# Performance work log

Measured on AMD Instinct MI355X. Metric: run time of the kernel, lower is better.

The kernel has to match this reference:

```python
import jax, jax.numpy as jnp
import numpy as np

RES = 1024
FEAT = 12
CB = 32
H_IMG, W_IMG = 1080, 1920


def cube_sample(cubemap, d):
    """Cube-map bilinear texture sample (nvdiffrast-style face selection,
    clamped bilinear within the selected face).
    cubemap: [6, R, R, C], d: [N, 3] unit directions -> [N, C]."""
    R = cubemap.shape[1]
    x, y, z = d[:, 0], d[:, 1], d[:, 2]
    ax, ay, az = jnp.abs(x), jnp.abs(y), jnp.abs(z)
    is_x = (ax >= ay) & (ax >= az)
    is_y = (~is_x) & (ay >= az)
    face = jnp.where(is_x, jnp.where(x >= 0, 0, 1),
           jnp.where(is_y, jnp.where(y >= 0, 2, 3),
                     jnp.where(z >= 0, 4, 5)))
    ma = jnp.where(is_x, ax, jnp.where(is_y, ay, az))
    u = jnp.where(is_x, jnp.where(x >= 0, -z, z),
        jnp.where(is_y, x, jnp.where(z >= 0, x, -x)))
    v = jnp.where(is_x, -y, jnp.where(is_y, jnp.where(y >= 0, z, -z), -y))
    eps = 1e-9
    s = (u / (ma + eps) + 1.0) * 0.5 * R - 0.5  # texel-space column
    t = (v / (ma + eps) + 1.0) * 0.5 * R - 0.5  # texel-space row
    x0 = jnp.floor(s); y0 = jnp.floor(t)
    fx = (s - x0)[:, None]; fy = (t - y0)[:, None]
    x0i = jnp.clip(x0.astype(jnp.int32), 0, R - 1)
    x1i = jnp.clip(x0i + 1, 0, R - 1)
    y0i = jnp.clip(y0.astype(jnp.int32), 0, R - 1)
    y1i = jnp.clip(y0i + 1, 0, R - 1)
    c00 = cubemap[face, y0i, x0i]
    c01 = cubemap[face, y0i, x1i]
    c10 = cubemap[face, y1i, x0i]
    c11 = cubemap[face, y1i, x1i]
    return (c00 * (1 - fx) + c01 * fx) * (1 - fy) + (c10 * (1 - fx) + c11 * fx) * fy


def setup_inputs() -> dict:
    key = jax.random.key(0)
    ks = jax.random.split(key, 9)
    rays_d = jax.random.normal(ks[0], (H_IMG, W_IMG, 3), jnp.float32)
    rays_d = rays_d / jnp.linalg.norm(rays_d, axis=-1, keepdims=True)
    mask = jax.random.randint(ks[1], (H_IMG, W_IMG), 0, 2) > 0  # sky mask
    sky_cube_map = jax.random.normal(ks[2], (6, RES, RES, FEAT), jnp.float32) * 0.1
    sky_codebook = jax.random.normal(ks[3], (CB, FEAT), jnp.float32) * 0.1
    W1 = jax.random.normal(ks[4], (FEAT + 3, 32), jnp.float32) * 0.25
    b1 = jnp.zeros((32,), jnp.float32)
    W2 = jax.random.normal(ks[5], (32, 32), jnp.float32) * 0.18
    b2 = jnp.zeros((32,), jnp.float32)
    W3 = jax.random.normal(ks[6], (32, 3), jnp.float32) * 0.18
    b3 = jnp.zeros((3,), jnp.float32)
    return {"rays_d": rays_d, "mask": mask, "sky_cube_map": sky_cube_map,
            "sky_codebook": sky_codebook, "W1": W1, "b1": b1,
            "W2": W2, "b2": b2, "W3": W3, "b3": b3}


def reference(rays_d, mask, sky_cube_map, sky_codebook, W1, b1, W2, b2, W3, b3):
    H, W = mask.shape
    d = rays_d.reshape(-1, 3)                       # [N, 3]
    feat_enc = cube_sample(sky_cube_map, d)         # [N, 12]
    # vq_st with detached codebook: nearest-codeword quantize, straight-through.
    cb = jax.lax.stop_gradient(sky_codebook)
    d2 = (jnp.sum(feat_enc * feat_enc, -1, keepdims=True)
          - 2.0 * (feat_enc @ cb.T)
          + jnp.sum(cb * cb, -1))                   # [N, 32]
    idx = jnp.argmin(d2, axis=-1)                   # [N]
    q = feat_enc + jax.lax.stop_gradient(cb[idx] - feat_enc)
    h = jnp.concatenate([q, d], axis=-1)            # [N, 15]
    h = jax.nn.relu(h @ W1 + b1)
    h = jax.nn.relu(h @ W2 + b2)
    rgb = jax.nn.sigmoid(h @ W3 + b3)               # [N, 3]
    # scatter shaded sky color into the (black-background) buffer via the mask
    img = jnp.where(mask.reshape(-1)[:, None], rgb, 0.0)
    return jnp.clip(img.reshape(H, W, 3).transpose(2, 0, 1), 0.0, 1.0)
```

## Files before the change

kernel.cpp:

```cpp
#include <hip/hip_runtime.h>
#include <math.h>

#define RES   1024
#define FEATC 12
#define CBN   32
#define H_IMG 1080
#define W_IMG 1920
#define NPIX  (H_IMG * W_IMG)

__global__ __launch_bounds__(256) void sky_kernel(
    const float* __restrict__ rays_d,
    const int*   __restrict__ mask,
    const float* __restrict__ cube,
    const float* __restrict__ cb,
    const float* __restrict__ W1,
    const float* __restrict__ b1,
    const float* __restrict__ W2,
    const float* __restrict__ b2,
    const float* __restrict__ W3,
    const float* __restrict__ b3,
    float*       __restrict__ out)
{
    __shared__ float sW1[15 * 32];
    __shared__ float sb1[32];
    __shared__ float sW2[32 * 32];
    __shared__ float sb2[32];
    __shared__ float sW3[32 * 3];
    __shared__ float sb3[3];
    __shared__ float sCB[CBN * FEATC];

    for (int t = threadIdx.x; t < 15 * 32; t += blockDim.x) sW1[t] = W1[t];
    for (int t = threadIdx.x; t < 32;      t += blockDim.x) sb1[t] = b1[t];
    for (int t = threadIdx.x; t < 32 * 32; t += blockDim.x) sW2[t] = W2[t];
    for (int t = threadIdx.x; t < 32;      t += blockDim.x) sb2[t] = b2[t];
    for (int t = threadIdx.x; t < 32 * 3;  t += blockDim.x) sW3[t] = W3[t];
    for (int t = threadIdx.x; t < 3;       t += blockDim.x) sb3[t] = b3[t];
    for (int t = threadIdx.x; t < CBN * FEATC; t += blockDim.x) sCB[t] = cb[t];
    __syncthreads();

    const int i = blockIdx.x * blockDim.x + threadIdx.x;
    if (i >= NPIX) return;

    if (mask[i] == 0) {
        out[0 * NPIX + i] = 0.0f;
        out[1 * NPIX + i] = 0.0f;
        out[2 * NPIX + i] = 0.0f;
        return;
    }

    const float x = rays_d[3 * i + 0];
    const float y = rays_d[3 * i + 1];
    const float z = rays_d[3 * i + 2];

    const float ax = fabsf(x), ay = fabsf(y), az = fabsf(z);
    const bool is_x = (ax >= ay) && (ax >= az);
    const bool is_y = (!is_x) && (ay >= az);

    int face; float ma, u, v;
    if (is_x) {
        face = (x >= 0.0f) ? 0 : 1;
        ma = ax;
        u = (x >= 0.0f) ? -z : z;
        v = -y;
    } else if (is_y) {
        face = (y >= 0.0f) ? 2 : 3;
        ma = ay;
        u = x;
        v = (y >= 0.0f) ? z : -z;
    } else {
        face = (z >= 0.0f) ? 4 : 5;
        ma = az;
        u = (z >= 0.0f) ? x : -x;
        v = -y;
    }

    const float denom = __fadd_rn(ma, 1e-9f);
    const float s = __fsub_rn(__fmul_rn(__fmul_rn(__fadd_rn(__fdiv_rn(u, denom), 1.0f), 0.5f), (float)RES), 0.5f);
    const float t = __fsub_rn(__fmul_rn(__fmul_rn(__fadd_rn(__fdiv_rn(v, denom), 1.0f), 0.5f), (float)RES), 0.5f);

    const float x0f = floorf(s);
    const float y0f = floorf(t);
    const float fx = __fsub_rn(s, x0f);
    const float fy = __fsub_rn(t, y0f);

    int x0i = (int)x0f; x0i = min(max(x0i, 0), RES - 1);
    int x1i = min(x0i + 1, RES - 1);
    int y0i = (int)y0f; y0i = min(max(y0i, 0), RES - 1);
    int y1i = min(y0i + 1, RES - 1);

    const size_t fbase = (size_t)face * RES * RES;
    const size_t off00 = (fbase + (size_t)y0i * RES + x0i) * FEATC;
    const size_t off01 = (fbase + (size_t)y0i * RES + x1i) * FEATC;
    const size_t off10 = (fbase + (size_t)y1i * RES + x0i) * FEATC;
    const size_t off11 = (fbase + (size_t)y1i * RES + x1i) * FEATC;

    const float4* p00 = (const float4*)(cube + off00);
    const float4* p01 = (const float4*)(cube + off01);
    const float4* p10 = (const float4*)(cube + off10);
    const float4* p11 = (const float4*)(cube + off11);

    float c00[FEATC], c01[FEATC], c10[FEATC], c11[FEATC];
    #pragma unroll
    for (int q4 = 0; q4 < 3; ++q4) {
        float4 a = p00[q4]; c00[4*q4+0]=a.x; c00[4*q4+1]=a.y; c00[4*q4+2]=a.z; c00[4*q4+3]=a.w;
        float4 b = p01[q4]; c01[4*q4+0]=b.x; c01[4*q4+1]=b.y; c01[4*q4+2]=b.z; c01[4*q4+3]=b.w;
        float4 c = p10[q4]; c10[4*q4+0]=c.x; c10[4*q4+1]=c.y; c10[4*q4+2]=c.z; c10[4*q4+3]=c.w;
        float4 dd= p11[q4]; c11[4*q4+0]=dd.x;c11[4*q4+1]=dd.y;c11[4*q4+2]=dd.z;c11[4*q4+3]=dd.w;
    }

    const float omfx = __fsub_rn(1.0f, fx);
    const float omfy = __fsub_rn(1.0f, fy);
    float feat[FEATC];
    #pragma unroll
    for (int k = 0; k < FEATC; ++k) {
        const float top = __fadd_rn(__fmul_rn(c00[k], omfx), __fmul_rn(c01[k], fx));
        const float bot = __fadd_rn(__fmul_rn(c10[k], omfx), __fmul_rn(c11[k], fx));
        feat[k] = __fadd_rn(__fmul_rn(top, omfy), __fmul_rn(bot, fy));
    }

    int best = 0;
    double bestd = 1e300;
    for (int j = 0; j < CBN; ++j) {
        double d2 = 0.0;
        #pragma unroll
        for (int k = 0; k < FEATC; ++k) {
            const double diff = (double)feat[k] - (double)sCB[j * FEATC + k];
            d2 += diff * diff;
        }
        if (d2 < bestd) { bestd = d2; best = j; }
    }

    float hin[15];
    #pragma unroll
    for (int k = 0; k < FEATC; ++k)
        hin[k] = __fadd_rn(feat[k], __fsub_rn(sCB[best * FEATC + k], feat[k]));
    hin[12] = x; hin[13] = y; hin[14] = z;

    float h1[32];
    #pragma unroll
    for (int k = 0; k < 32; ++k) {
        float a = sb1[k];
        #pragma unroll
        for (int j = 0; j < 15; ++j) a += hin[j] * sW1[j * 32 + k];
        h1[k] = fmaxf(a, 0.0f);
    }

    float h2[32];
    #pragma unroll
    for (int k = 0; k < 32; ++k) {
        float a = sb2[k];
        #pragma unroll
        for (int j = 0; j < 32; ++j) a += h1[j] * sW2[j * 32 + k];
        h2[k] = fmaxf(a, 0.0f);
    }

    #pragma unroll
    for (int c = 0; c < 3; ++c) {
        float a = sb3[c];
        #pragma unroll
        for (int j = 0; j < 32; ++j) a += h2[j] * sW3[j * 3 + c];
        float r = 1.0f / (1.0f + expf(-a));
        r = fminf(fmaxf(r, 0.0f), 1.0f);
        out[(size_t)c * NPIX + i] = r;
    }
}

extern "C" void kernel_launch(void* const* d_in, const int* in_sizes, int n_in,
                              void* d_out, int out_size, void* d_ws, size_t ws_size,
                              hipStream_t stream) {
    const float* rays_d = (const float*)d_in[0];
    const int*   mask   = (const int*)d_in[1];
    const float* cube   = (const float*)d_in[2];
    const float* cb     = (const float*)d_in[3];
    const float* W1     = (const float*)d_in[4];
    const float* b1     = (const float*)d_in[5];
    const float* W2     = (const float*)d_in[6];
    const float* b2     = (const float*)d_in[7];
    const float* W3     = (const float*)d_in[8];
    const float* b3     = (const float*)d_in[9];
    float* out = (float*)d_out;

    const int block = 256;
    const int grid = (NPIX + block - 1) / block;
    sky_kernel<<<grid, block, 0, stream>>>(rays_d, mask, cube, cb,
                                           W1, b1, W2, b2, W3, b3, out);
}
```

Before: 618.2 us.

## Compact masked pixels into an active list before shading to remove divergence

Adds a prep pass that zeroes background pixels and appends active pixel indices to a workspace list using a global atomic counter. A persistent grid-stride kernel then shades only the listed pixels, so wavefronts no longer idle on half-masked lanes. The codebook search is also changed to a dot-product form with precomputed squared norms in double, and the MLP loops are reordered to an outer-product style. The costs are two extra launches, heavy contention on a single atomic, loss of memory coalescing because list order is scrambled, and a possible change in argmin tie behaviour.

```diff
diff --git a/kernel.cpp b/kernel.cpp
--- a/kernel.cpp
+++ b/kernel.cpp
@@ -8,26 +8,180 @@
 #define W_IMG 1920
 #define NPIX  (H_IMG * W_IMG)
 
-__global__ __launch_bounds__(256) void sky_kernel(
+
+__device__ __forceinline__ void face_uv(float x, float y, float z,
+                                        int& face, float& ma, float& u, float& v)
+{
+    const float ax = fabsf(x), ay = fabsf(y), az = fabsf(z);
+    const bool is_x = (ax >= ay) && (ax >= az);
+    const bool is_y = (!is_x) && (ay >= az);
+    if (is_x) {
+        face = (x >= 0.0f) ? 0 : 1;
+        ma = ax; u = (x >= 0.0f) ? -z : z; v = -y;
+    } else if (is_y) {
+        face = (y >= 0.0f) ? 2 : 3;
+        ma = ay; u = x; v = (y >= 0.0f) ? z : -z;
+    } else {
+        face = (z >= 0.0f) ? 4 : 5;
+        ma = az; u = (z >= 0.0f) ? x : -x; v = -y;
+    }
+}
+
+__device__ __forceinline__ void shade_pixel(
+    int i,
     const float* __restrict__ rays_d,
-    const int*   __restrict__ mask,
+    const float* __restrict__ cube,
+    const float* sW1, const float* sb1,
+    const float* sW2, const float* sb2,
+    const float* sW3, const float* sb3,
+    const float* sCB, const double* sCN,
+    float* __restrict__ out)
+{
+    const float x = rays_d[3 * i + 0];
+    const float y = rays_d[3 * i + 1];
+    const float z = rays_d[3 * i + 2];
+
+    int face; float ma, u, v;
+    face_uv(x, y, z, face, ma, u, v);
+
+    const float denom = __fadd_rn(ma, 1e-9f);
+    const float s = __fsub_rn(__fmul_rn(__fmul_rn(__fadd_rn(__fdiv_rn(u, denom), 1.0f), 0.5f), (float)RES), 0.5f);
+    const float t = __fsub_rn(__fmul_rn(__fmul_rn(__fadd_rn(__fdiv_rn(v, denom), 1.0f), 0.5f), (float)RES), 0.5f);
+
+    const float x0f = floorf(s);
+    const float y0f = floorf(t);
+    const float fx = __fsub_rn(s, x0f);
+    const float fy = __fsub_rn(t, y0f);
+
+    int x0i = (int)x0f; x0i = min(max(x0i, 0), RES - 1);
+    int x1i = min(x0i + 1, RES - 1);
+    int y0i = (int)y0f; y0i = min(max(y0i, 0), RES - 1);
+    int y1i = min(y0i + 1, RES - 1);
+
+    const size_t fbase = (size_t)face * RES * RES;
+    const float4* p00 = (const float4*)(cube + (fbase + (size_t)y0i * RES + x0i) * FEATC);
+    const float4* p01 = (const float4*)(cube + (fbase + (size_t)y0i * RES + x1i) * FEATC);
+    const float4* p10 = (const float4*)(cube + (fbase + (size_t)y1i * RES + x0i) * FEATC);
+    const float4* p11 = (const float4*)(cube + (fbase + (size_t)y1i * RES + x1i) * FEATC);
+
+    float c00[FEATC], c01[FEATC], c10[FEATC], c11[FEATC];
+    #pragma unroll
+    for (int q4 = 0; q4 < 3; ++q4) {
+        float4 a = p00[q4]; c00[4*q4+0]=a.x; c00[4*q4+1]=a.y; c00[4*q4+2]=a.z; c00[4*q4+3]=a.w;
+        float4 b = p01[q4]; c01[4*q4+0]=b.x; c01[4*q4+1]=b.y; c01[4*q4+2]=b.z; c01[4*q4+3]=b.w;
+        float4 c = p10[q4]; c10[4*q4+0]=c.x; c10[4*q4+1]=c.y; c10[4*q4+2]=c.z; c10[4*q4+3]=c.w;
+        float4 dd= p11[q4]; c11[4*q4+0]=dd.x;c11[4*q4+1]=dd.y;c11[4*q4+2]=dd.z;c11[4*q4+3]=dd.w;
+    }
+
+    const float omfx = __fsub_rn(1.0f, fx);
+    const float omfy = __fsub_rn(1.0f, fy);
+    float feat[FEATC];
+    double featd[FEATC];
+    #pragma unroll
+    for (int k = 0; k < FEATC; ++k) {
+        const float top = __fadd_rn(__fmul_rn(c00[k], omfx), __fmul_rn(c01[k], fx));
+        const float bot = __fadd_rn(__fmul_rn(c10[k], omfx), __fmul_rn(c11[k], fx));
+        feat[k] = __fadd_rn(__fmul_rn(top, omfy), __fmul_rn(bot, fy));
+        featd[k] = (double)feat[k];
+    }
+
+    int best = 0;
+    double bestd = 1e300;
+    for (int j = 0; j < CBN; ++j) {
+        double dot = 0.0;
+        #pragma unroll
+        for (int k = 0; k < FEATC; ++k)
+            dot = fma(featd[k], (double)sCB[j * FEATC + k], dot);
+        const double d2 = fma(-2.0, dot, sCN[j]);
+        if (d2 < bestd) { bestd = d2; best = j; }
+    }
+
+    float hin[15];
+    #pragma unroll
+    for (int k = 0; k < FEATC; ++k)
+        hin[k] = __fadd_rn(feat[k], __fsub_rn(sCB[best * FEATC + k], feat[k]));
+    hin[12] = x; hin[13] = y; hin[14] = z;
+
+    float h1[32];
+    #pragma unroll
+    for (int k = 0; k < 32; ++k) h1[k] = sb1[k];
+    #pragma unroll
+    for (int j = 0; j < 15; ++j) {
+        const float a = hin[j];
+        #pragma unroll
+        for (int k = 0; k < 32; ++k) h1[k] += a * sW1[j * 32 + k];
+    }
+    #pragma unroll
+    for (int k = 0; k < 32; ++k) h1[k] = fmaxf(h1[k], 0.0f);
+
+    float h2[32];
+    #pragma unroll
+    for (int k = 0; k < 32; ++k) h2[k] = sb2[k];
+    #pragma unroll
+    for (int j = 0; j < 32; ++j) {
+        const float a = h1[j];
+        #pragma unroll
+        for (int k = 0; k < 32; ++k) h2[k] += a * sW2[j * 32 + k];
+    }
+    #pragma unroll
+    for (int k = 0; k < 32; ++k) h2[k] = fmaxf(h2[k], 0.0f);
+
+    #pragma unroll
+    for (int c = 0; c < 3; ++c) {
+        float a = sb3[c];
+        #pragma unroll
+        for (int j = 0; j < 32; ++j) a += h2[j] * sW3[j * 3 + c];
+        float r = 1.0f / (1.0f + expf(-a));
+        r = fminf(fmaxf(r, 0.0f), 1.0f);
+        out[(size_t)c * NPIX + i] = r;
+    }
+}
+
+
+__global__ void zero_counter(int* __restrict__ counter) {
+    if (threadIdx.x == 0 && blockIdx.x == 0) *counter = 0;
+}
+
+
+__global__ __launch_bounds__(256) void prep_kernel(
+    const int* __restrict__ mask,
+    float*     __restrict__ out,
+    int*       __restrict__ counter,
+    int*       __restrict__ list)
+{
+    const int i = blockIdx.x * blockDim.x + threadIdx.x;
+    if (i >= NPIX) return;
+    const bool active = (mask[i] != 0);
+    if (!active) {
+        out[0 * NPIX + i] = 0.0f;
+        out[1 * NPIX + i] = 0.0f;
+        out[2 * NPIX + i] = 0.0f;
+    } else {
+        const int pos = atomicAdd(counter, 1);
+        list[pos] = i;
+    }
+}
+
+
+__global__ __launch_bounds__(256) void sky_main(
+    const float* __restrict__ rays_d,
     const float* __restrict__ cube,
     const float* __restrict__ cb,
-    const float* __restrict__ W1,
-    const float* __restrict__ b1,
-    const float* __restrict__ W2,
-    const float* __restrict__ b2,
-    const float* __restrict__ W3,
-    const float* __restrict__ b3,
+    const float* __restrict__ W1, const float* __restrict__ b1,
+    const float* __restrict__ W2, const float* __restrict__ b2,
+    const float* __restrict__ W3, const float* __restrict__ b3,
+    const int*   __restrict__ counter,
+    const int*   __restrict__ list,
     float*       __restrict__ out)
 {
-    __shared__ float sW1[15 * 32];
-    __shared__ float sb1[32];
-    __shared__ float sW2[32 * 32];
-    __shared__ float sb2[32];
-    __shared__ float sW3[32 * 3];
-    __shared__ float sb3[3];
-    __shared__ float sCB[CBN * FEATC];
+    __shared__ float  sW1[15 * 32];
+    __shared__ float  sb1[32];
+    __shared__ float  sW2[32 * 32];
+    __shared__ float  sb2[32];
+    __shared__ float  sW3[32 * 3];
+    __shared__ float  sb3[3];
+    __shared__ float  sCB[CBN * FEATC];
+    __shared__ double sCN[CBN];
 
     for (int t = threadIdx.x; t < 15 * 32; t += blockDim.x) sW1[t] = W1[t];
     for (int t = threadIdx.x; t < 32;      t += blockDim.x) sb1[t] = b1[t];
@@ -36,134 +190,74 @@
     for (int t = threadIdx.x; t < 32 * 3;  t += blockDim.x) sW3[t] = W3[t];
     for (int t = threadIdx.x; t < 3;       t += blockDim.x) sb3[t] = b3[t];
     for (int t = threadIdx.x; t < CBN * FEATC; t += blockDim.x) sCB[t] = cb[t];
+    if (threadIdx.x < CBN) {
+        double sum = 0.0;
+        #pragma unroll
+        for (int k = 0; k < FEATC; ++k) {
+            const double c = (double)cb[threadIdx.x * FEATC + k];
+            sum = fma(c, c, sum);
+        }
+        sCN[threadIdx.x] = sum;
+    }
+    __syncthreads();
+
+    const int total = *counter;
+    const int stride = gridDim.x * blockDim.x;
+    for (int t = blockIdx.x * blockDim.x + threadIdx.x; t < total; t += stride) {
+        const int i = list[t];
+        shade_pixel(i, rays_d, cube, sW1, sb1, sW2, sb2, sW3, sb3, sCB, sCN, out);
+    }
+}
+
+
+__global__ __launch_bounds__(256) void sky_mono(
+    const float* __restrict__ rays_d,
+    const int*   __restrict__ mask,
+    const float* __restrict__ cube,
+    const float* __restrict__ cb,
+    const float* __restrict__ W1, const float* __restrict__ b1,
+    const float* __restrict__ W2, const float* __restrict__ b2,
+    const float* __restrict__ W3, const float* __restrict__ b3,
+    float*       __restrict__ out)
+{
+    __shared__ float  sW1[15 * 32];
+    __shared__ float  sb1[32];
+    __shared__ float  sW2[32 * 32];
+    __shared__ float  sb2[32];
+    __shared__ float  sW3[32 * 3];
+    __shared__ float  sb3[3];
+    __shared__ float  sCB[CBN * FEATC];
+    __shared__ double sCN[CBN];
+
+    for (int t = threadIdx.x; t < 15 * 32; t += blockDim.x) sW1[t] = W1[t];
+    for (int t = threadIdx.x; t < 32;      t += blockDim.x) sb1[t] = b1[t];
+    for (int t = threadIdx.x; t < 32 * 32; t += blockDim.x) sW2[t] = W2[t];
+    for (int t = threadIdx.x; t < 32;      t += blockDim.x) sb2[t] = b2[t];
+    for (int t = threadIdx.x; t < 32 * 3;  t += blockDim.x) sW3[t] = W3[t];
+    for (int t = threadIdx.x; t < 3;       t += blockDim.x) sb3[t] = b3[t];
+    for (int t = threadIdx.x; t < CBN * FEATC; t += blockDim.x) sCB[t] = cb[t];
+    if (threadIdx.x < CBN) {
+        double sum = 0.0;
+        #pragma unroll
+        for (int k = 0; k < FEATC; ++k) {
+            const double c = (double)cb[threadIdx.x * FEATC + k];
+            sum = fma(c, c, sum);
+        }
+        sCN[threadIdx.x] = sum;
+    }
     __syncthreads();
 
     const int i = blockIdx.x * blockDim.x + threadIdx.x;
     if (i >= NPIX) return;
-
     if (mask[i] == 0) {
         out[0 * NPIX + i] = 0.0f;
         out[1 * NPIX + i] = 0.0f;
         out[2 * NPIX + i] = 0.0f;
         return;
     }
-
-    const float x = rays_d[3 * i + 0];
-    const float y = rays_d[3 * i + 1];
-    const float z = rays_d[3 * i + 2];
-
-    const float ax = fabsf(x), ay = fabsf(y), az = fabsf(z);
-    const bool is_x = (ax >= ay) && (ax >= az);
-    const bool is_y = (!is_x) && (ay >= az);
-
-    int face; float ma, u, v;
-    if (is_x) {
-        face = (x >= 0.0f) ? 0 : 1;
-        ma = ax;
-        u = (x >= 0.0f) ? -z : z;
-        v = -y;
-    } else if (is_y) {
-        face = (y >= 0.0f) ? 2 : 3;
-        ma = ay;
-        u = x;
-        v = (y >= 0.0f) ? z : -z;
-    } else {
-        face = (z >= 0.0f) ? 4 : 5;
-        ma = az;
-        u = (z >= 0.0f) ? x : -x;
-        v = -y;
-    }
-
-    const float denom = __fadd_rn(ma, 1e-9f);
-    const float s = __fsub_rn(__fmul_rn(__fmul_rn(__fadd_rn(__fdiv_rn(u, denom), 1.0f), 0.5f), (float)RES), 0.5f);
-    const float t = __fsub_rn(__fmul_rn(__fmul_rn(__fadd_rn(__fdiv_rn(v, denom), 1.0f), 0.5f), (float)RES), 0.5f);
-
-    const float x0f = floorf(s);
-    const float y0f = floorf(t);
-    const float fx = __fsub_rn(s, x0f);
-    const float fy = __fsub_rn(t, y0f);
-
-    int x0i = (int)x0f; x0i = min(max(x0i, 0), RES - 1);
-    int x1i = min(x0i + 1, RES - 1);
-    int y0i = (int)y0f; y0i = min(max(y0i, 0), RES - 1);
-    int y1i = min(y0i + 1, RES - 1);
-
-    const size_t fbase = (size_t)face * RES * RES;
-    const size_t off00 = (fbase + (size_t)y0i * RES + x0i) * FEATC;
-    const size_t off01 = (fbase + (size_t)y0i * RES + x1i) * FEATC;
-    const size_t off10 = (fbase + (size_t)y1i * RES + x0i) * FEATC;
-    const size_t off11 = (fbase + (size_t)y1i * RES + x1i) * FEATC;
-
-    const float4* p00 = (const float4*)(cube + off00);
-    const float4* p01 = (const float4*)(cube + off01);
-    const float4* p10 = (const float4*)(cube + off10);
-    const float4* p11 = (const float4*)(cube + off11);
-
-    float c00[FEATC], c01[FEATC], c10[FEATC], c11[FEATC];
-    #pragma unroll
-    for (int q4 = 0; q4 < 3; ++q4) {
-        float4 a = p00[q4]; c00[4*q4+0]=a.x; c00[4*q4+1]=a.y; c00[4*q4+2]=a.z; c00[4*q4+3]=a.w;
-        float4 b = p01[q4]; c01[4*q4+0]=b.x; c01[4*q4+1]=b.y; c01[4*q4+2]=b.z; c01[4*q4+3]=b.w;
-        float4 c = p10[q4]; c10[4*q4+0]=c.x; c10[4*q4+1]=c.y; c10[4*q4+2]=c.z; c10[4*q4+3]=c.w;
-        float4 dd= p11[q4]; c11[4*q4+0]=dd.x;c11[4*q4+1]=dd.y;c11[4*q4+2]=dd.z;c11[4*q4+3]=dd.w;
-    }
-
-    const float omfx = __fsub_rn(1.0f, fx);
-    const float omfy = __fsub_rn(1.0f, fy);
-    float feat[FEATC];
-    #pragma unroll
-    for (int k = 0; k < FEATC; ++k) {
-        const float top = __fadd_rn(__fmul_rn(c00[k], omfx), __fmul_rn(c01[k], fx));
-        const float bot = __fadd_rn(__fmul_rn(c10[k], omfx), __fmul_rn(c11[k], fx));
-        feat[k] = __fadd_rn(__fmul_rn(top, omfy), __fmul_rn(bot, fy));
-    }
-
-    int best = 0;
-    double bestd = 1e300;
-    for (int j = 0; j < CBN; ++j) {
-        double d2 = 0.0;
-        #pragma unroll
-        for (int k = 0; k < FEATC; ++k) {
-            const double diff = (double)feat[k] - (double)sCB[j * FEATC + k];
-            d2 += diff * diff;
-        }
-        if (d2 < bestd) { bestd = d2; best = j; }
-    }
-
-    float hin[15];
-    #pragma unroll
-    for (int k = 0; k < FEATC; ++k)
-        hin[k] = __fadd_rn(feat[k], __fsub_rn(sCB[best * FEATC + k], feat[k]));
-    hin[12] = x; hin[13] = y; hin[14] = z;
-
-    float h1[32];
-    #pragma unroll
-    for (int k = 0; k < 32; ++k) {
-        float a = sb1[k];
-        #pragma unroll
-        for (int j = 0; j < 15; ++j) a += hin[j] * sW1[j * 32 + k];
-        h1[k] = fmaxf(a, 0.0f);
-    }
-
-    float h2[32];
-    #pragma unroll
-    for (int k = 0; k < 32; ++k) {
-        float a = sb2[k];
-        #pragma unroll
-        for (int j = 0; j < 32; ++j) a += h1[j] * sW2[j * 32 + k];
-        h2[k] = fmaxf(a, 0.0f);
-    }
-
-    #pragma unroll
-    for (int c = 0; c < 3; ++c) {
-        float a = sb3[c];
-        #pragma unroll
-        for (int j = 0; j < 32; ++j) a += h2[j] * sW3[j * 3 + c];
-        float r = 1.0f / (1.0f + expf(-a));
-        r = fminf(fmaxf(r, 0.0f), 1.0f);
-        out[(size_t)c * NPIX + i] = r;
-    }
-}
+    shade_pixel(i, rays_d, cube, sW1, sb1, sW2, sb2, sW3, sb3, sCB, sCN, out);
+}
+
 
 extern "C" void kernel_launch(void* const* d_in, const int* in_sizes, int n_in,
                               void* d_out, int out_size, void* d_ws, size_t ws_size,
@@ -180,8 +274,25 @@
     const float* b3     = (const float*)d_in[9];
     float* out = (float*)d_out;
 
+    const size_t ws_needed = 16 + (size_t)NPIX * sizeof(int);
     const int block = 256;
-    const int grid = (NPIX + block - 1) / block;
-    sky_kernel<<<grid, block, 0, stream>>>(rays_d, mask, cube, cb,
-                                           W1, b1, W2, b2, W3, b3, out);
-}
+
+    if (ws_size >= ws_needed) {
+        int* counter = (int*)d_ws;
+        int* list    = (int*)((char*)d_ws + 16);
+
+        zero_counter<<<1, 64, 0, stream>>>(counter);
+
+        const int gridA = (NPIX + block - 1) / block;
+        prep_kernel<<<gridA, block, 0, stream>>>(mask, out, counter, list);
+
+        const int gridB = 4096;
+        sky_main<<<gridB, block, 0, stream>>>(rays_d, cube, cb,
+                                              W1, b1, W2, b2, W3, b3,
+                                              counter, list, out);
+    } else {
+        const int grid = (NPIX + block - 1) / block;
+        sky_mono<<<grid, block, 0, stream>>>(rays_d, mask, cube, cb,
+                                             W1, b1, W2, b2, W3, b3, out);
+    }
+}
```

After: 1.129 ms. 82.6% more time.

## Compact active sky pixels per block to remove masked-lane divergence

Applied to the files above, without the earlier changes.

Each block now handles a 2048-pixel segment: it reads the mask, writes zeros for inactive pixels, and builds a compacted list of active pixel indices in shared memory using wave ballots and per-wave prefix sums. Threads then shade only the listed pixels, so wavefronts stay fully occupied instead of half their lanes idling on the random 50% mask. The cost is extra barriers during compaction, 8 KB more shared memory per block, and scattered pixel ordering, which loses coalescing on the rays_d loads and output stores.

```diff
diff --git a/kernel.cpp b/kernel.cpp
--- a/kernel.cpp
+++ b/kernel.cpp
@@ -7,18 +7,133 @@
 #define H_IMG 1080
 #define W_IMG 1920
 #define NPIX  (H_IMG * W_IMG)
-
-__global__ __launch_bounds__(256) void sky_kernel(
+#define SEG   2048
+#define PPT   (SEG / 256)
+
+__device__ __forceinline__ void shade_pixel(
+    int i,
+    const float* __restrict__ rays_d,
+    const float* __restrict__ cube,
+    const float* sW1, const float* sb1,
+    const float* sW2, const float* sb2,
+    const float* sW3, const float* sb3,
+    const float* sCB,
+    float* __restrict__ out)
+{
+    const float x = rays_d[3 * i + 0];
+    const float y = rays_d[3 * i + 1];
+    const float z = rays_d[3 * i + 2];
+
+    const float ax = fabsf(x), ay = fabsf(y), az = fabsf(z);
+    const bool is_x = (ax >= ay) && (ax >= az);
+    const bool is_y = (!is_x) && (ay >= az);
+
+    int face; float ma, u, v;
+    if (is_x) {
+        face = (x >= 0.0f) ? 0 : 1;
+        ma = ax; u = (x >= 0.0f) ? -z : z; v = -y;
+    } else if (is_y) {
+        face = (y >= 0.0f) ? 2 : 3;
+        ma = ay; u = x; v = (y >= 0.0f) ? z : -z;
+    } else {
+        face = (z >= 0.0f) ? 4 : 5;
+        ma = az; u = (z >= 0.0f) ? x : -x; v = -y;
+    }
+
+    const float denom = __fadd_rn(ma, 1e-9f);
+    const float s = __fsub_rn(__fmul_rn(__fmul_rn(__fadd_rn(__fdiv_rn(u, denom), 1.0f), 0.5f), (float)RES), 0.5f);
+    const float t = __fsub_rn(__fmul_rn(__fmul_rn(__fadd_rn(__fdiv_rn(v, denom), 1.0f), 0.5f), (float)RES), 0.5f);
+
+    const float x0f = floorf(s);
+    const float y0f = floorf(t);
+    const float fx = __fsub_rn(s, x0f);
+    const float fy = __fsub_rn(t, y0f);
+
+    int x0i = (int)x0f; x0i = min(max(x0i, 0), RES - 1);
+    int x1i = min(x0i + 1, RES - 1);
+    int y0i = (int)y0f; y0i = min(max(y0i, 0), RES - 1);
+    int y1i = min(y0i + 1, RES - 1);
+
+    const size_t fbase = (size_t)face * RES * RES;
+    const float4* p00 = (const float4*)(cube + (fbase + (size_t)y0i * RES + x0i) * FEATC);
+    const float4* p01 = (const float4*)(cube + (fbase + (size_t)y0i * RES + x1i) * FEATC);
+    const float4* p10 = (const float4*)(cube + (fbase + (size_t)y1i * RES + x0i) * FEATC);
+    const float4* p11 = (const float4*)(cube + (fbase + (size_t)y1i * RES + x1i) * FEATC);
+
+    float c00[FEATC], c01[FEATC], c10[FEATC], c11[FEATC];
+    #pragma unroll
+    for (int q4 = 0; q4 < 3; ++q4) {
+        float4 a = p00[q4]; c00[4*q4+0]=a.x; c00[4*q4+1]=a.y; c00[4*q4+2]=a.z; c00[4*q4+3]=a.w;
+        float4 b = p01[q4]; c01[4*q4+0]=b.x; c01[4*q4+1]=b.y; c01[4*q4+2]=b.z; c01[4*q4+3]=b.w;
+        float4 c = p10[q4]; c10[4*q4+0]=c.x; c10[4*q4+1]=c.y; c10[4*q4+2]=c.z; c10[4*q4+3]=c.w;
+        float4 dd= p11[q4]; c11[4*q4+0]=dd.x;c11[4*q4+1]=dd.y;c11[4*q4+2]=dd.z;c11[4*q4+3]=dd.w;
+    }
+
+    const float omfx = __fsub_rn(1.0f, fx);
+    const float omfy = __fsub_rn(1.0f, fy);
+    float feat[FEATC];
+    #pragma unroll
+    for (int k = 0; k < FEATC; ++k) {
+        const float top = __fadd_rn(__fmul_rn(c00[k], omfx), __fmul_rn(c01[k], fx));
+        const float bot = __fadd_rn(__fmul_rn(c10[k], omfx), __fmul_rn(c11[k], fx));
+        feat[k] = __fadd_rn(__fmul_rn(top, omfy), __fmul_rn(bot, fy));
+    }
+
+    int best = 0;
+    double bestd = 1e300;
+    for (int j = 0; j < CBN; ++j) {
+        double d2 = 0.0;
+        #pragma unroll
+        for (int k = 0; k < FEATC; ++k) {
+            const double diff = (double)feat[k] - (double)sCB[j * FEATC + k];
+            d2 += diff * diff;
+        }
+        if (d2 < bestd) { bestd = d2; best = j; }
+    }
+
+    float hin[15];
+    #pragma unroll
+    for (int k = 0; k < FEATC; ++k)
+        hin[k] = __fadd_rn(feat[k], __fsub_rn(sCB[best * FEATC + k], feat[k]));
+    hin[12] = x; hin[13] = y; hin[14] = z;
+
+    float h1[32];
+    #pragma unroll
+    for (int k = 0; k < 32; ++k) {
+        float a = sb1[k];
+        #pragma unroll
+        for (int j = 0; j < 15; ++j) a += hin[j] * sW1[j * 32 + k];
+        h1[k] = fmaxf(a, 0.0f);
+    }
+
+    float h2[32];
+    #pragma unroll
+    for (int k = 0; k < 32; ++k) {
+        float a = sb2[k];
+        #pragma unroll
+        for (int j = 0; j < 32; ++j) a += h1[j] * sW2[j * 32 + k];
+        h2[k] = fmaxf(a, 0.0f);
+    }
+
+    #pragma unroll
+    for (int c = 0; c < 3; ++c) {
+        float a = sb3[c];
+        #pragma unroll
+        for (int j = 0; j < 32; ++j) a += h2[j] * sW3[j * 3 + c];
+        float r = 1.0f / (1.0f + expf(-a));
+        r = fminf(fmaxf(r, 0.0f), 1.0f);
+        out[(size_t)c * NPIX + i] = r;
+    }
+}
+
+__global__ __launch_bounds__(256) void sky_fused(
     const float* __restrict__ rays_d,
     const int*   __restrict__ mask,
     const float* __restrict__ cube,
     const float* __restrict__ cb,
-    const float* __restrict__ W1,
-    const float* __restrict__ b1,
-    const float* __restrict__ W2,
-    const float* __restrict__ b2,
-    const float* __restrict__ W3,
-    const float* __restrict__ b3,
+    const float* __restrict__ W1, const float* __restrict__ b1,
+    const float* __restrict__ W2, const float* __restrict__ b2,
+    const float* __restrict__ W3, const float* __restrict__ b3,
     float*       __restrict__ out)
 {
     __shared__ float sW1[15 * 32];
@@ -28,6 +143,8 @@
     __shared__ float sW3[32 * 3];
     __shared__ float sb3[3];
     __shared__ float sCB[CBN * FEATC];
+    __shared__ int   sList[SEG];
+    __shared__ int   sWsum[4];
 
     for (int t = threadIdx.x; t < 15 * 32; t += blockDim.x) sW1[t] = W1[t];
     for (int t = threadIdx.x; t < 32;      t += blockDim.x) sb1[t] = b1[t];
@@ -38,130 +155,39 @@
     for (int t = threadIdx.x; t < CBN * FEATC; t += blockDim.x) sCB[t] = cb[t];
     __syncthreads();
 
-    const int i = blockIdx.x * blockDim.x + threadIdx.x;
-    if (i >= NPIX) return;
-
-    if (mask[i] == 0) {
-        out[0 * NPIX + i] = 0.0f;
-        out[1 * NPIX + i] = 0.0f;
-        out[2 * NPIX + i] = 0.0f;
-        return;
-    }
-
-    const float x = rays_d[3 * i + 0];
-    const float y = rays_d[3 * i + 1];
-    const float z = rays_d[3 * i + 2];
-
-    const float ax = fabsf(x), ay = fabsf(y), az = fabsf(z);
-    const bool is_x = (ax >= ay) && (ax >= az);
-    const bool is_y = (!is_x) && (ay >= az);
-
-    int face; float ma, u, v;
-    if (is_x) {
-        face = (x >= 0.0f) ? 0 : 1;
-        ma = ax;
-        u = (x >= 0.0f) ? -z : z;
-        v = -y;
-    } else if (is_y) {
-        face = (y >= 0.0f) ? 2 : 3;
-        ma = ay;
-        u = x;
-        v = (y >= 0.0f) ? z : -z;
-    } else {
-        face = (z >= 0.0f) ? 4 : 5;
-        ma = az;
-        u = (z >= 0.0f) ? x : -x;
-        v = -y;
-    }
-
-    const float denom = __fadd_rn(ma, 1e-9f);
-    const float s = __fsub_rn(__fmul_rn(__fmul_rn(__fadd_rn(__fdiv_rn(u, denom), 1.0f), 0.5f), (float)RES), 0.5f);
-    const float t = __fsub_rn(__fmul_rn(__fmul_rn(__fadd_rn(__fdiv_rn(v, denom), 1.0f), 0.5f), (float)RES), 0.5f);
-
-    const float x0f = floorf(s);
-    const float y0f = floorf(t);
-    const float fx = __fsub_rn(s, x0f);
-    const float fy = __fsub_rn(t, y0f);
-
-    int x0i = (int)x0f; x0i = min(max(x0i, 0), RES - 1);
-    int x1i = min(x0i + 1, RES - 1);
-    int y0i = (int)y0f; y0i = min(max(y0i, 0), RES - 1);
-    int y1i = min(y0i + 1, RES - 1);
-
-    const size_t fbase = (size_t)face * RES * RES;
-    const size_t off00 = (fbase + (size_t)y0i * RES + x0i) * FEATC;
-    const size_t off01 = (fbase + (size_t)y0i * RES + x1i) * FEATC;
-    const size_t off10 = (fbase + (size_t)y1i * RES + x0i) * FEATC;
-    const size_t off11 = (fbase + (size_t)y1i * RES + x1i) * FEATC;
-
-    const float4* p00 = (const float4*)(cube + off00);
-    const float4* p01 = (const float4*)(cube + off01);
-    const float4* p10 = (const float4*)(cube + off10);
-    const float4* p11 = (const float4*)(cube + off11);
-
-    float c00[FEATC], c01[FEATC], c10[FEATC], c11[FEATC];
-    #pragma unroll
-    for (int q4 = 0; q4 < 3; ++q4) {
-        float4 a = p00[q4]; c00[4*q4+0]=a.x; c00[4*q4+1]=a.y; c00[4*q4+2]=a.z; c00[4*q4+3]=a.w;
-        float4 b = p01[q4]; c01[4*q4+0]=b.x; c01[4*q4+1]=b.y; c01[4*q4+2]=b.z; c01[4*q4+3]=b.w;
-        float4 c = p10[q4]; c10[4*q4+0]=c.x; c10[4*q4+1]=c.y; c10[4*q4+2]=c.z; c10[4*q4+3]=c.w;
-        float4 dd= p11[q4]; c11[4*q4+0]=dd.x;c11[4*q4+1]=dd.y;c11[4*q4+2]=dd.z;c11[4*q4+3]=dd.w;
-    }
-
-    const float omfx = __fsub_rn(1.0f, fx);
-    const float omfy = __fsub_rn(1.0f, fy);
-    float feat[FEATC];
-    #pragma unroll
-    for (int k = 0; k < FEATC; ++k) {
-        const float top = __fadd_rn(__fmul_rn(c00[k], omfx), __fmul_rn(c01[k], fx));
-        const float bot = __fadd_rn(__fmul_rn(c10[k], omfx), __fmul_rn(c11[k], fx));
-        feat[k] = __fadd_rn(__fmul_rn(top, omfy), __fmul_rn(bot, fy));
-    }
-
-    int best = 0;
-    double bestd = 1e300;
-    for (int j = 0; j < CBN; ++j) {
-        double d2 = 0.0;
-        #pragma unroll
-        for (int k = 0; k < FEATC; ++k) {
-            const double diff = (double)feat[k] - (double)sCB[j * FEATC + k];
-            d2 += diff * diff;
+    const int tid  = threadIdx.x;
+    const int lane = tid & 63;
+    const int wid  = tid >> 6;
+    const int seg0 = blockIdx.x * SEG;
+
+    int nAct = 0;
+    #pragma unroll
+    for (int r = 0; r < PPT; ++r) {
+        const int i = seg0 + r * 256 + tid;
+        bool act = false;
+        if (i < NPIX) {
+            act = (mask[i] != 0);
+            if (!act) {
+                out[0 * NPIX + i] = 0.0f;
+                out[1 * NPIX + i] = 0.0f;
+                out[2 * NPIX + i] = 0.0f;
+            }
         }
-        if (d2 < bestd) { bestd = d2; best = j; }
-    }
-
-    float hin[15];
-    #pragma unroll
-    for (int k = 0; k < FEATC; ++k)
-        hin[k] = __fadd_rn(feat[k], __fsub_rn(sCB[best * FEATC + k], feat[k]));
-    hin[12] = x; hin[13] = y; hin[14] = z;
-
-    float h1[32];
-    #pragma unroll
-    for (int k = 0; k < 32; ++k) {
-        float a = sb1[k];
-        #pragma unroll
-        for (int j = 0; j < 15; ++j) a += hin[j] * sW1[j * 32 + k];
-        h1[k] = fmaxf(a, 0.0f);
-    }
-
-    float h2[32];
-    #pragma unroll
-    for (int k = 0; k < 32; ++k) {
-        float a = sb2[k];
-        #pragma unroll
-        for (int j = 0; j < 32; ++j) a += h1[j] * sW2[j * 32 + k];
-        h2[k] = fmaxf(a, 0.0f);
-    }
-
-    #pragma unroll
-    for (int c = 0; c < 3; ++c) {
-        float a = sb3[c];
-        #pragma unroll
-        for (int j = 0; j < 32; ++j) a += h2[j] * sW3[j * 3 + c];
-        float r = 1.0f / (1.0f + expf(-a));
-        r = fminf(fmaxf(r, 0.0f), 1.0f);
-        out[(size_t)c * NPIX + i] = r;
+        const unsigned long long bal = __ballot(act);
+        const int rank = __popcll(bal & ((1ull << lane) - 1ull));
+        if (lane == 0) sWsum[wid] = (int)__popcll(bal);
+        __syncthreads();
+        int woff = 0;
+        #pragma unroll
+        for (int w = 0; w < 4; ++w) woff += (w < wid) ? sWsum[w] : 0;
+        const int wtot = sWsum[0] + sWsum[1] + sWsum[2] + sWsum[3];
+        if (act) sList[nAct + woff + rank] = i;
+        nAct += wtot;
+        __syncthreads();
+    }
+
+    for (int t = tid; t < nAct; t += 256) {
+        shade_pixel(sList[t], rays_d, cube, sW1, sb1, sW2, sb2, sW3, sb3, sCB, out);
     }
 }
 
@@ -180,8 +206,7 @@
     const float* b3     = (const float*)d_in[9];
     float* out = (float*)d_out;
 
-    const int block = 256;
-    const int grid = (NPIX + block - 1) / block;
-    sky_kernel<<<grid, block, 0, stream>>>(rays_d, mask, cube, cb,
-                                           W1, b1, W2, b2, W3, b3, out);
+    const int grid = (NPIX + SEG - 1) / SEG;
+    sky_fused<<<grid, 256, 0, stream>>>(rays_d, mask, cube, cb,
+                                        W1, b1, W2, b2, W3, b3, out);
 }
```

New measurement: 771.0 us. 1.25x slower.
